# Kernel tuning notes

Measured on AMD Instinct MI355X. Metric: run time of the kernel, lower is better.

The kernel has to match this reference:

```python
import jax, jax.numpy as jnp
import numpy as np

DIM = 768
HEADS = 12
B, N = 1, 4096


def setup_inputs() -> dict:
    key = jax.random.key(0)
    k1, k2, k3 = jax.random.split(key, 3)
    x = jax.random.normal(k1, (B, N, DIM), dtype=jnp.float32)
    W_qkv = jax.random.normal(k2, (DIM, 3 * DIM), dtype=jnp.float32) * (DIM ** -0.5)
    W_out = jax.random.normal(k3, (DIM, DIM), dtype=jnp.float32) * (DIM ** -0.5)
    b_out = jnp.zeros((DIM,), dtype=jnp.float32)
    return {"x": x, "W_qkv": W_qkv, "W_out": W_out, "b_out": b_out}


def reference(x, W_qkv, W_out, b_out):
    b, n, dim = x.shape
    h = HEADS
    d = dim // h
    qkv = x @ W_qkv  # [b, n, 3*dim]
    q, k, v = jnp.split(qkv, 3, axis=-1)
    # 'b n (h d) -> b h n d'
    def to_heads(a):
        return a.reshape(b, n, h, d).transpose(0, 2, 1, 3)
    q, k, v = to_heads(q), to_heads(k), to_heads(v)
    # NOTE: original module computes self.scale but never applies it -> unscaled dots
    dots = jnp.einsum('bhid,bhjd->bhij', q, k)
    attn = jax.nn.softmax(dots, axis=-1)
    out = jnp.einsum('bhij,bhjd->bhid', attn, v)
    out = out.transpose(0, 2, 1, 3).reshape(b, n, dim)  # 'b h n d -> b n (h d)'
    return out @ W_out + b_out
```

## Files before the change

### kernel.cpp

```cpp
#include <hip/hip_runtime.h>

typedef unsigned short ushort_t;
typedef unsigned int uint_t;
typedef __bf16 bf16x8 __attribute__((ext_vector_type(8)));
typedef __bf16 bf16x4 __attribute__((ext_vector_type(4)));
typedef float f32x4 __attribute__((ext_vector_type(4)));
typedef ushort_t u16x4 __attribute__((ext_vector_type(4)));

#define NSEQ 4096
#define DIMM 768
#define NQKV 2304
#define HEADS 12
#define LOG2E 1.4426950408889634f

#if __has_builtin(__builtin_amdgcn_exp2f)
#define EXP2(x) __builtin_amdgcn_exp2f(x)
#else
#define EXP2(x) exp2f(x)
#endif


__device__ __forceinline__ ushort_t f2bf(float f) {
    uint_t u = __float_as_uint(f);
    u = u + 0x7fffu + ((u >> 16) & 1u);
    return (ushort_t)(u >> 16);
}
__device__ __forceinline__ f32x4 zero4() {
    f32x4 v = {0.f, 0.f, 0.f, 0.f};
    return v;
}

__global__ __launch_bounds__(256) void cvt_x_pack_kernel(const float* __restrict__ src,
                                                         ushort_t* __restrict__ dst) {
    int i = blockIdx.x * 256 + threadIdx.x;
    int row = i / (DIMM / 4);
    int k0 = (i - row * (DIMM / 4)) * 4;
    float4 v = *(const float4*)(&src[(size_t)row * DIMM + k0]);
    u16x4 p = { f2bf(v.x), f2bf(v.y), f2bf(v.z), f2bf(v.w) };
    size_t idx = ((size_t)(row >> 4) * (DIMM / 8) + (k0 >> 3)) * 128 + (row & 15) * 8 + (k0 & 7);
    *(u16x4*)(&dst[idx]) = p;
}

__global__ __launch_bounds__(256) void pack_w_kernel(
    const float* __restrict__ src, ushort_t* __restrict__ dst, int K, int N)
{
    __shared__ ushort_t Ls[64 * 72];
    const int t = threadIdx.x;
    const int bk = blockIdx.x * 64;
    const int bn = blockIdx.y * 64;
    const int tr = t >> 4, tc = t & 15;
#pragma unroll
    for (int i = 0; i < 4; ++i) {
        int r = tr + 16 * i;
        float4 v = *(const float4*)(&src[(size_t)(bk + r) * N + bn + tc * 4]);
        const float* vv = (const float*)&v;
#pragma unroll
        for (int j = 0; j < 4; ++j) Ls[(tc * 4 + j) * 72 + r] = f2bf(vv[j]);
    }
    __syncthreads();
    const int KB = K >> 3;
    const int n = t >> 2;
    const int ks = t & 3;
    const int gn = bn + n;
    size_t base = ((size_t)(gn >> 4) * KB + ((bk + ks * 16) >> 3)) * 128 + (gn & 15) * 8;
    *(uint4*)(&dst[base])       = *(const uint4*)(&Ls[n * 72 + ks * 16]);
    *(uint4*)(&dst[base + 128]) = *(const uint4*)(&Ls[n * 72 + ks * 16 + 8]);
}

__global__ __launch_bounds__(256) void qkv_gemm_kernel(
    const ushort_t* __restrict__ Ap, const ushort_t* __restrict__ Bp,
    ushort_t* __restrict__ Qp, ushort_t* __restrict__ Kp, ushort_t* __restrict__ Vp)
{
    const int t = threadIdx.x;
    const int lane = t & 63;
    const int w = t >> 6;
    const int m16 = lane & 15;
    const int g = lane >> 4;
    const int wrow = (w >> 1) * 64;
    const int wcol = (w & 1) * 64;
    const int bm = blockIdx.y * 128;
    const int bn = blockIdx.x * 128;
    const int amb = (bm + wrow) >> 4;
    const int bnb = (bn + wcol) >> 4;
    const int KB = DIMM / 8;
    const int which = bn / DIMM;

    f32x4 acc[4][4];
#pragma unroll
    for (int i = 0; i < 4; ++i)
#pragma unroll
        for (int j = 0; j < 4; ++j) acc[i][j] = zero4();

    if (which < 2) {
#pragma unroll 2
        for (int kt = 0; kt < 24; ++kt) {
            bf16x8 af[4], bfv[4];
#pragma unroll
            for (int mi = 0; mi < 4; ++mi)
                af[mi] = *(const bf16x8*)(&Ap[((size_t)(amb + mi) * KB + kt * 4 + g) * 128 + m16 * 8]);
#pragma unroll
            for (int nj = 0; nj < 4; ++nj)
                bfv[nj] = *(const bf16x8*)(&Bp[((size_t)(bnb + nj) * KB + kt * 4 + g) * 128 + m16 * 8]);
#pragma unroll
            for (int mi = 0; mi < 4; ++mi)
#pragma unroll
                for (int nj = 0; nj < 4; ++nj)
                    acc[mi][nj] = __builtin_amdgcn_mfma_f32_16x16x32_bf16(bfv[nj], af[mi], acc[mi][nj], 0, 0, 0);
        }
        ushort_t* dst = (which == 0) ? Qp : Kp;
        const float scale = (which == 0) ? LOG2E : 1.0f;
        const int cb = bn - which * DIMM + wcol;
        const int h = cb >> 6;
        const int ghi = g >> 1, glo = g & 1;
#pragma unroll
        for (int mi = 0; mi < 4; ++mi) {
            int sblk = amb + mi;
#pragma unroll
            for (int nj = 0; nj < 4; ++nj) {
                size_t idx = (((size_t)h * 256 + sblk) * 8 + nj * 2 + ghi) * 128 + m16 * 8 + glo * 4;
                u16x4 pk = { f2bf(acc[mi][nj][0] * scale), f2bf(acc[mi][nj][1] * scale),
                             f2bf(acc[mi][nj][2] * scale), f2bf(acc[mi][nj][3] * scale) };
                *(u16x4*)(&dst[idx]) = pk;
            }
        }
    } else {
#pragma unroll 2
        for (int kt = 0; kt < 24; ++kt) {
            bf16x8 af[4], bfv[4];
#pragma unroll
            for (int mi = 0; mi < 4; ++mi)
                af[mi] = *(const bf16x8*)(&Ap[((size_t)(amb + mi) * KB + kt * 4 + g) * 128 + m16 * 8]);
#pragma unroll
            for (int nj = 0; nj < 4; ++nj)
                bfv[nj] = *(const bf16x8*)(&Bp[((size_t)(bnb + nj) * KB + kt * 4 + g) * 128 + m16 * 8]);
#pragma unroll
            for (int mi = 0; mi < 4; ++mi)
#pragma unroll
                for (int nj = 0; nj < 4; ++nj)
                    acc[mi][nj] = __builtin_amdgcn_mfma_f32_16x16x32_bf16(af[mi], bfv[nj], acc[mi][nj], 0, 0, 0);
        }
        const int cb = bn - 2 * DIMM + wcol;
        const int h = cb >> 6;
        const int ghi = g >> 1, glo = g & 1;
        const int kb8 = (bm + wrow) >> 3;
#pragma unroll
        for (int mi = 0; mi < 4; ++mi) {
#pragma unroll
            for (int nj = 0; nj < 4; ++nj) {
                size_t idx = (((size_t)h * 512 + kb8 + mi * 2 + ghi) * 4 + nj) * 128 + m16 * 8 + glo * 4;
                u16x4 pk = { f2bf(acc[mi][nj][0]), f2bf(acc[mi][nj][1]),
                             f2bf(acc[mi][nj][2]), f2bf(acc[mi][nj][3]) };
                *(u16x4*)(&Vp[idx]) = pk;
            }
        }
    }
}

__global__ __launch_bounds__(256, 2) void attn_kernel(
    const ushort_t* __restrict__ Qp, const ushort_t* __restrict__ Kp,
    const ushort_t* __restrict__ Vp, float* __restrict__ Opart, float* __restrict__ Lpart,
    int niter)
{
    __shared__ ushort_t Ps[4][32 * 72];
    const int t = threadIdx.x;
    const int lane = t & 63;
    const int w = t >> 6;
    const int m16 = lane & 15;
    const int g = lane >> 4;
    const int h = blockIdx.y;
    const int half = blockIdx.z;
    const int qb = blockIdx.x * 128 + w * 32;
    const int qblk0 = qb >> 4;
    const int kblk0 = half * niter * 4;
    const int vblk0 = half * niter * 8;

    bf16x8 qf[2][2];
#pragma unroll
    for (int mi = 0; mi < 2; ++mi)
#pragma unroll
        for (int kd = 0; kd < 2; ++kd)
            qf[mi][kd] = *(const bf16x8*)(&Qp[(((size_t)h * 256 + qblk0 + mi) * 8 + kd * 4 + g) * 128 + m16 * 8]);

    const ushort_t* kpA = Kp + ((size_t)h * 256 + kblk0) * 1024 + g * 128 + m16 * 8;
    const ushort_t* kpB = kpA + 2048;
    const ushort_t* vpA = Vp + ((size_t)h * 512 + vblk0) * 512 + g * 512 + m16 * 8;
    const ushort_t* vpB = vpA + 2048;

    f32x4 oacc[2][4];
#pragma unroll
    for (int mi = 0; mi < 2; ++mi)
#pragma unroll
        for (int dj = 0; dj < 4; ++dj) oacc[mi][dj] = zero4();
    f32x4 lacc[2] = {zero4(), zero4()};

#pragma unroll 4
    for (int kt = 0; kt < niter; ++kt) {
        bf16x8 kf[4][2];
        kf[0][0] = *(const bf16x8*)(kpA);
        kf[0][1] = *(const bf16x8*)(kpA + 512);
        kf[1][0] = *(const bf16x8*)(kpA + 1024);
        kf[1][1] = *(const bf16x8*)(kpA + 1536);
        kf[2][0] = *(const bf16x8*)(kpB);
        kf[2][1] = *(const bf16x8*)(kpB + 512);
        kf[3][0] = *(const bf16x8*)(kpB + 1024);
        kf[3][1] = *(const bf16x8*)(kpB + 1536);
        bf16x8 vf[4][2];
#pragma unroll
        for (int dj = 0; dj < 4; ++dj) {
            vf[dj][0] = *(const bf16x8*)(vpA + dj * 128);
            vf[dj][1] = *(const bf16x8*)(vpB + dj * 128);
        }
        kpA += 4096; kpB += 4096; vpA += 4096; vpB += 4096;

#pragma unroll
        for (int nj = 0; nj < 4; ++nj) {
#pragma unroll
            for (int mi = 0; mi < 2; ++mi) {
                f32x4 st = zero4();
#pragma unroll
                for (int kd = 0; kd < 2; ++kd)
                    st = __builtin_amdgcn_mfma_f32_16x16x32_bf16(kf[nj][kd], qf[mi][kd], st, 0, 0, 0);
                f32x4 p;
#pragma unroll
                for (int r = 0; r < 4; ++r) p[r] = EXP2(st[r]);
                lacc[mi] += p;
                bf16x4 pk = { (__bf16)p[0], (__bf16)p[1], (__bf16)p[2], (__bf16)p[3] };
                *(bf16x4*)(&Ps[w][(mi * 16 + m16) * 72 + nj * 16 + g * 4]) = pk;
            }
        }
        bf16x8 pf[2][2];
#pragma unroll
        for (int mi = 0; mi < 2; ++mi)
#pragma unroll
            for (int kc = 0; kc < 2; ++kc)
                pf[mi][kc] = *(const bf16x8*)(&Ps[w][(mi * 16 + m16) * 72 + kc * 32 + g * 8]);
#pragma unroll
        for (int mi = 0; mi < 2; ++mi)
#pragma unroll
            for (int dj = 0; dj < 4; ++dj)
#pragma unroll
                for (int kc = 0; kc < 2; ++kc)
                    oacc[mi][dj] = __builtin_amdgcn_mfma_f32_16x16x32_bf16(pf[mi][kc], vf[dj][kc], oacc[mi][dj], 0, 0, 0);
    }

    float* Oph = Opart + (size_t)half * NSEQ * DIMM;
    float* Lph = Lpart + (size_t)half * HEADS * NSEQ + (size_t)h * NSEQ;
#pragma unroll
    for (int mi = 0; mi < 2; ++mi) {
        float l = (lacc[mi][0] + lacc[mi][1]) + (lacc[mi][2] + lacc[mi][3]);
        l += __shfl_xor(l, 16);
        l += __shfl_xor(l, 32);
        if (g == 0) Lph[qb + mi * 16 + m16] = l;
    }
#pragma unroll
    for (int mi = 0; mi < 2; ++mi) {
#pragma unroll
        for (int r = 0; r < 4; ++r) {
            int row = qb + mi * 16 + g * 4 + r;
#pragma unroll
            for (int dj = 0; dj < 4; ++dj)
                Oph[(size_t)row * DIMM + h * 64 + dj * 16 + m16] = oacc[mi][dj][r];
        }
    }
}

__global__ __launch_bounds__(256) void merge_kernel(
    const float* __restrict__ Opart, const float* __restrict__ Lpart,
    ushort_t* __restrict__ Xap, int nsplit)
{
    int i = blockIdx.x * 256 + threadIdx.x;
    int row = i / (DIMM / 4);
    int col0 = (i - row * (DIMM / 4)) * 4;
    int h = col0 >> 6;
    float l = 0.f;
    f32x4 o = zero4();
    for (int s = 0; s < nsplit; ++s) {
        l += Lpart[(size_t)s * HEADS * NSEQ + (size_t)h * NSEQ + row];
        f32x4 ov = *(const f32x4*)(&Opart[(size_t)s * NSEQ * DIMM + (size_t)row * DIMM + col0]);
        o += ov;
    }
    float inv = 1.0f / l;
    u16x4 p = { f2bf(o[0] * inv), f2bf(o[1] * inv), f2bf(o[2] * inv), f2bf(o[3] * inv) };
    size_t idx = ((size_t)(row >> 4) * (DIMM / 8) + (col0 >> 3)) * 128 + (row & 15) * 8 + (col0 & 7);
    *(u16x4*)(&Xap[idx]) = p;
}

__global__ __launch_bounds__(128) void out_gemm_kernel(
    const ushort_t* __restrict__ Ap, const ushort_t* __restrict__ Bp,
    const float* __restrict__ bias, float* __restrict__ out)
{
    const int t = threadIdx.x;
    const int lane = t & 63;
    const int w = t >> 6;
    const int m16 = lane & 15;
    const int g = lane >> 4;
    const int bm = blockIdx.y * 128;
    const int bn = blockIdx.x * 64;
    const int amb = (bm + w * 64) >> 4;
    const int bnb = bn >> 4;
    const int KB = DIMM / 8;

    f32x4 acc[4][4];
#pragma unroll
    for (int i = 0; i < 4; ++i)
#pragma unroll
        for (int j = 0; j < 4; ++j) acc[i][j] = zero4();

#pragma unroll 2
    for (int kt = 0; kt < 24; ++kt) {
        bf16x8 af[4], bfv[4];
#pragma unroll
        for (int mi = 0; mi < 4; ++mi)
            af[mi] = *(const bf16x8*)(&Ap[((size_t)(amb + mi) * KB + kt * 4 + g) * 128 + m16 * 8]);
#pragma unroll
        for (int nj = 0; nj < 4; ++nj)
            bfv[nj] = *(const bf16x8*)(&Bp[((size_t)(bnb + nj) * KB + kt * 4 + g) * 128 + m16 * 8]);
#pragma unroll
        for (int mi = 0; mi < 4; ++mi)
#pragma unroll
            for (int nj = 0; nj < 4; ++nj)
                acc[mi][nj] = __builtin_amdgcn_mfma_f32_16x16x32_bf16(af[mi], bfv[nj], acc[mi][nj], 0, 0, 0);
    }
#pragma unroll
    for (int mi = 0; mi < 4; ++mi) {
#pragma unroll
        for (int nj = 0; nj < 4; ++nj) {
            int col = bn + nj * 16 + m16;
            float bv = bias[col];
#pragma unroll
            for (int r = 0; r < 4; ++r) {
                int row = bm + w * 64 + mi * 16 + g * 4 + r;
                out[(size_t)row * DIMM + col] = acc[mi][nj][r] + bv;
            }
        }
    }
}

extern "C" void kernel_launch(void* const* d_in, const int* in_sizes, int n_in,
                              void* d_out, int out_size, void* d_ws, size_t ws_size,
                              hipStream_t stream) {
    (void)in_sizes; (void)n_in; (void)out_size;
    const float* X    = (const float*)d_in[0];
    const float* Wqkv = (const float*)d_in[1];
    const float* Wout = (const float*)d_in[2];
    const float* bout = (const float*)d_in[3];
    float* out = (float*)d_out;

    const size_t TSZ = (size_t)NSEQ * DIMM;
    const size_t fixed = TSZ * 2 * 5 + (size_t)NQKV * DIMM * 2 + (size_t)DIMM * DIMM * 2;
    const size_t per_split = TSZ * 4 + (size_t)HEADS * NSEQ * 4;
    const int nsplit = (ws_size >= fixed + 4 * per_split) ? 4 : 2;

    unsigned char* p = (unsigned char*)d_ws;
    ushort_t* Ap  = (ushort_t*)p; p += TSZ * 2;
    ushort_t* Wqp = (ushort_t*)p; p += (size_t)NQKV * DIMM * 2;
    ushort_t* Wop = (ushort_t*)p; p += (size_t)DIMM * DIMM * 2;
    ushort_t* Qp  = (ushort_t*)p; p += TSZ * 2;
    ushort_t* Kp  = (ushort_t*)p; p += TSZ * 2;
    ushort_t* Vp  = (ushort_t*)p; p += TSZ * 2;
    ushort_t* Xap = (ushort_t*)p; p += TSZ * 2;
    float* Opart  = (float*)p;    p += (size_t)nsplit * TSZ * 4;
    float* Lpart  = (float*)p;

    const int niter = (NSEQ / 64) / nsplit;

    cvt_x_pack_kernel<<<TSZ / 4 / 256, 256, 0, stream>>>(X, Ap);
    pack_w_kernel<<<dim3(DIMM / 64, NQKV / 64), 256, 0, stream>>>(Wqkv, Wqp, DIMM, NQKV);
    pack_w_kernel<<<dim3(DIMM / 64, DIMM / 64), 256, 0, stream>>>(Wout, Wop, DIMM, DIMM);
    qkv_gemm_kernel<<<dim3(NQKV / 128, NSEQ / 128), 256, 0, stream>>>(Ap, Wqp, Qp, Kp, Vp);
    attn_kernel<<<dim3(NSEQ / 128, HEADS, nsplit), 256, 0, stream>>>(Qp, Kp, Vp, Opart, Lpart, niter);
    merge_kernel<<<TSZ / 4 / 256, 256, 0, stream>>>(Opart, Lpart, Xap, nsplit);
    out_gemm_kernel<<<dim3(DIMM / 64, NSEQ / 128), 128, 0, stream>>>(Xap, Wop, bout, out);
}
```

Measured before the change: 210.5 us.

## Fuse prep kernels, widen GEMM warp tiles, use single-wave attention blocks with fixed split

```diff
diff --git a/kernel.cpp b/kernel.cpp
--- a/kernel.cpp
+++ b/kernel.cpp
@@ -30,24 +30,10 @@
     return v;
 }
 
-__global__ __launch_bounds__(256) void cvt_x_pack_kernel(const float* __restrict__ src,
-                                                         ushort_t* __restrict__ dst) {
-    int i = blockIdx.x * 256 + threadIdx.x;
-    int row = i / (DIMM / 4);
-    int k0 = (i - row * (DIMM / 4)) * 4;
-    float4 v = *(const float4*)(&src[(size_t)row * DIMM + k0]);
-    u16x4 p = { f2bf(v.x), f2bf(v.y), f2bf(v.z), f2bf(v.w) };
-    size_t idx = ((size_t)(row >> 4) * (DIMM / 8) + (k0 >> 3)) * 128 + (row & 15) * 8 + (k0 & 7);
-    *(u16x4*)(&dst[idx]) = p;
-}
-
-__global__ __launch_bounds__(256) void pack_w_kernel(
-    const float* __restrict__ src, ushort_t* __restrict__ dst, int K, int N)
-{
-    __shared__ ushort_t Ls[64 * 72];
-    const int t = threadIdx.x;
-    const int bk = blockIdx.x * 64;
-    const int bn = blockIdx.y * 64;
+__device__ __forceinline__ void pack_w_tile(const float* __restrict__ src,
+                                            ushort_t* __restrict__ dst,
+                                            int K, int N, int bk, int bn, int t,
+                                            ushort_t* Ls) {
     const int tr = t >> 4, tc = t & 15;
 #pragma unroll
     for (int i = 0; i < 4; ++i) {
@@ -67,7 +53,44 @@
     *(uint4*)(&dst[base + 128]) = *(const uint4*)(&Ls[n * 72 + ks * 16 + 8]);
 }
 
-__global__ __launch_bounds__(256) void qkv_gemm_kernel(
+#define CVT_BLOCKS   3072
+#define PW1_BLOCKS   (12 * 36)
+#define PW2_BLOCKS   (12 * 12)
+
+__global__ __launch_bounds__(256) void prep_kernel(
+    const float* __restrict__ X, const float* __restrict__ Wqkv, const float* __restrict__ Wout,
+    ushort_t* __restrict__ Ap, ushort_t* __restrict__ Wqp, ushort_t* __restrict__ Wop)
+{
+    __shared__ ushort_t Ls[64 * 72];
+    const int b = blockIdx.x;
+    const int t = threadIdx.x;
+    if (b < CVT_BLOCKS) {
+        int i = b * 256 + t;
+        int row = i / (DIMM / 4);
+        int k0 = (i - row * (DIMM / 4)) * 4;
+        float4 v = *(const float4*)(&X[(size_t)row * DIMM + k0]);
+        u16x4 p = { f2bf(v.x), f2bf(v.y), f2bf(v.z), f2bf(v.w) };
+        size_t idx = ((size_t)(row >> 4) * (DIMM / 8) + (k0 >> 3)) * 128 + (row & 15) * 8 + (k0 & 7);
+        *(u16x4*)(&Ap[idx]) = p;
+    } else if (b < CVT_BLOCKS + PW1_BLOCKS) {
+        int j = b - CVT_BLOCKS;
+        pack_w_tile(Wqkv, Wqp, DIMM, NQKV, (j % 12) * 64, (j / 12) * 64, t, Ls);
+    } else {
+        int j = b - CVT_BLOCKS - PW1_BLOCKS;
+        pack_w_tile(Wout, Wop, DIMM, DIMM, (j % 12) * 64, (j / 12) * 64, t, Ls);
+    }
+}
+
+#define QKV_LOAD8(af, bfv, kt) do {                                                           \
+    _Pragma("unroll")                                                                         \
+    for (int mi = 0; mi < 4; ++mi)                                                            \
+        af[mi] = *(const bf16x8*)(&Ap[((size_t)(amb + mi) * KB + (kt) * 4 + g) * 128 + m16 * 8]); \
+    _Pragma("unroll")                                                                         \
+    for (int nj = 0; nj < 8; ++nj)                                                            \
+        bfv[nj] = *(const bf16x8*)(&Bp[((size_t)(bnb + nj) * KB + (kt) * 4 + g) * 128 + m16 * 8]); \
+} while (0)
+
+__global__ __launch_bounds__(128, 2) void qkv_gemm_kernel(
     const ushort_t* __restrict__ Ap, const ushort_t* __restrict__ Bp,
     ushort_t* __restrict__ Qp, ushort_t* __restrict__ Kp, ushort_t* __restrict__ Vp)
 {
@@ -76,78 +99,64 @@
     const int w = t >> 6;
     const int m16 = lane & 15;
     const int g = lane >> 4;
-    const int wrow = (w >> 1) * 64;
-    const int wcol = (w & 1) * 64;
-    const int bm = blockIdx.y * 128;
-    const int bn = blockIdx.x * 128;
-    const int amb = (bm + wrow) >> 4;
+    const int bm = blockIdx.y * 64;
+    const int bn = blockIdx.x * 256;
+    const int wcol = w * 128;
+    const int amb = bm >> 4;
     const int bnb = (bn + wcol) >> 4;
     const int KB = DIMM / 8;
     const int which = bn / DIMM;
-
-    f32x4 acc[4][4];
+    const int ghi = g >> 1, glo = g & 1;
+
+    f32x4 acc[4][8];
 #pragma unroll
     for (int i = 0; i < 4; ++i)
 #pragma unroll
-        for (int j = 0; j < 4; ++j) acc[i][j] = zero4();
+        for (int j = 0; j < 8; ++j) acc[i][j] = zero4();
 
     if (which < 2) {
-#pragma unroll 2
         for (int kt = 0; kt < 24; ++kt) {
-            bf16x8 af[4], bfv[4];
+            bf16x8 af[4], bfv[8];
+            QKV_LOAD8(af, bfv, kt);
 #pragma unroll
             for (int mi = 0; mi < 4; ++mi)
-                af[mi] = *(const bf16x8*)(&Ap[((size_t)(amb + mi) * KB + kt * 4 + g) * 128 + m16 * 8]);
-#pragma unroll
-            for (int nj = 0; nj < 4; ++nj)
-                bfv[nj] = *(const bf16x8*)(&Bp[((size_t)(bnb + nj) * KB + kt * 4 + g) * 128 + m16 * 8]);
-#pragma unroll
-            for (int mi = 0; mi < 4; ++mi)
-#pragma unroll
-                for (int nj = 0; nj < 4; ++nj)
+#pragma unroll
+                for (int nj = 0; nj < 8; ++nj)
                     acc[mi][nj] = __builtin_amdgcn_mfma_f32_16x16x32_bf16(bfv[nj], af[mi], acc[mi][nj], 0, 0, 0);
         }
         ushort_t* dst = (which == 0) ? Qp : Kp;
         const float scale = (which == 0) ? LOG2E : 1.0f;
         const int cb = bn - which * DIMM + wcol;
-        const int h = cb >> 6;
-        const int ghi = g >> 1, glo = g & 1;
 #pragma unroll
         for (int mi = 0; mi < 4; ++mi) {
             int sblk = amb + mi;
 #pragma unroll
-            for (int nj = 0; nj < 4; ++nj) {
-                size_t idx = (((size_t)h * 256 + sblk) * 8 + nj * 2 + ghi) * 128 + m16 * 8 + glo * 4;
+            for (int nj = 0; nj < 8; ++nj) {
+                int h = (cb >> 6) + (nj >> 2);
+                size_t idx = (((size_t)h * 256 + sblk) * 8 + (nj & 3) * 2 + ghi) * 128 + m16 * 8 + glo * 4;
                 u16x4 pk = { f2bf(acc[mi][nj][0] * scale), f2bf(acc[mi][nj][1] * scale),
                              f2bf(acc[mi][nj][2] * scale), f2bf(acc[mi][nj][3] * scale) };
                 *(u16x4*)(&dst[idx]) = pk;
             }
         }
     } else {
-#pragma unroll 2
         for (int kt = 0; kt < 24; ++kt) {
-            bf16x8 af[4], bfv[4];
+            bf16x8 af[4], bfv[8];
+            QKV_LOAD8(af, bfv, kt);
 #pragma unroll
             for (int mi = 0; mi < 4; ++mi)
-                af[mi] = *(const bf16x8*)(&Ap[((size_t)(amb + mi) * KB + kt * 4 + g) * 128 + m16 * 8]);
-#pragma unroll
-            for (int nj = 0; nj < 4; ++nj)
-                bfv[nj] = *(const bf16x8*)(&Bp[((size_t)(bnb + nj) * KB + kt * 4 + g) * 128 + m16 * 8]);
-#pragma unroll
-            for (int mi = 0; mi < 4; ++mi)
-#pragma unroll
-                for (int nj = 0; nj < 4; ++nj)
+#pragma unroll
+                for (int nj = 0; nj < 8; ++nj)
                     acc[mi][nj] = __builtin_amdgcn_mfma_f32_16x16x32_bf16(af[mi], bfv[nj], acc[mi][nj], 0, 0, 0);
         }
         const int cb = bn - 2 * DIMM + wcol;
-        const int h = cb >> 6;
-        const int ghi = g >> 1, glo = g & 1;
-        const int kb8 = (bm + wrow) >> 3;
+        const int kb8 = bm >> 3;
 #pragma unroll
         for (int mi = 0; mi < 4; ++mi) {
 #pragma unroll
-            for (int nj = 0; nj < 4; ++nj) {
-                size_t idx = (((size_t)h * 512 + kb8 + mi * 2 + ghi) * 4 + nj) * 128 + m16 * 8 + glo * 4;
+            for (int nj = 0; nj < 8; ++nj) {
+                int h = (cb >> 6) + (nj >> 2);
+                size_t idx = (((size_t)h * 512 + kb8 + mi * 2 + ghi) * 4 + (nj & 3)) * 128 + m16 * 8 + glo * 4;
                 u16x4 pk = { f2bf(acc[mi][nj][0]), f2bf(acc[mi][nj][1]),
                              f2bf(acc[mi][nj][2]), f2bf(acc[mi][nj][3]) };
                 *(u16x4*)(&Vp[idx]) = pk;
@@ -156,27 +165,25 @@
     }
 }
 
-__global__ __launch_bounds__(256, 2) void attn_kernel(
+__global__ __launch_bounds__(64, 2) void attn_kernel(
     const ushort_t* __restrict__ Qp, const ushort_t* __restrict__ Kp,
     const ushort_t* __restrict__ Vp, float* __restrict__ Opart, float* __restrict__ Lpart,
     int niter)
 {
-    __shared__ ushort_t Ps[4][32 * 72];
-    const int t = threadIdx.x;
-    const int lane = t & 63;
-    const int w = t >> 6;
+    __shared__ ushort_t Ps[64 * 72];
+    const int lane = threadIdx.x & 63;
     const int m16 = lane & 15;
     const int g = lane >> 4;
     const int h = blockIdx.y;
     const int half = blockIdx.z;
-    const int qb = blockIdx.x * 128 + w * 32;
+    const int qb = blockIdx.x * 64;
     const int qblk0 = qb >> 4;
     const int kblk0 = half * niter * 4;
     const int vblk0 = half * niter * 8;
 
-    bf16x8 qf[2][2];
-#pragma unroll
-    for (int mi = 0; mi < 2; ++mi)
+    bf16x8 qf[4][2];
+#pragma unroll
+    for (int mi = 0; mi < 4; ++mi)
 #pragma unroll
         for (int kd = 0; kd < 2; ++kd)
             qf[mi][kd] = *(const bf16x8*)(&Qp[(((size_t)h * 256 + qblk0 + mi) * 8 + kd * 4 + g) * 128 + m16 * 8]);
@@ -186,14 +193,13 @@
     const ushort_t* vpA = Vp + ((size_t)h * 512 + vblk0) * 512 + g * 512 + m16 * 8;
     const ushort_t* vpB = vpA + 2048;
 
-    f32x4 oacc[2][4];
-#pragma unroll
-    for (int mi = 0; mi < 2; ++mi)
+    f32x4 oacc[4][4];
+#pragma unroll
+    for (int mi = 0; mi < 4; ++mi)
 #pragma unroll
         for (int dj = 0; dj < 4; ++dj) oacc[mi][dj] = zero4();
-    f32x4 lacc[2] = {zero4(), zero4()};
-
-#pragma unroll 4
+    f32x4 lacc[4] = {zero4(), zero4(), zero4(), zero4()};
+
     for (int kt = 0; kt < niter; ++kt) {
         bf16x8 kf[4][2];
         kf[0][0] = *(const bf16x8*)(kpA);
@@ -215,45 +221,41 @@
 #pragma unroll
         for (int nj = 0; nj < 4; ++nj) {
 #pragma unroll
-            for (int mi = 0; mi < 2; ++mi) {
+            for (int mi = 0; mi < 4; ++mi) {
                 f32x4 st = zero4();
-#pragma unroll
-                for (int kd = 0; kd < 2; ++kd)
-                    st = __builtin_amdgcn_mfma_f32_16x16x32_bf16(kf[nj][kd], qf[mi][kd], st, 0, 0, 0);
+                st = __builtin_amdgcn_mfma_f32_16x16x32_bf16(kf[nj][0], qf[mi][0], st, 0, 0, 0);
+                st = __builtin_amdgcn_mfma_f32_16x16x32_bf16(kf[nj][1], qf[mi][1], st, 0, 0, 0);
                 f32x4 p;
 #pragma unroll
                 for (int r = 0; r < 4; ++r) p[r] = EXP2(st[r]);
                 lacc[mi] += p;
                 bf16x4 pk = { (__bf16)p[0], (__bf16)p[1], (__bf16)p[2], (__bf16)p[3] };
-                *(bf16x4*)(&Ps[w][(mi * 16 + m16) * 72 + nj * 16 + g * 4]) = pk;
-            }
-        }
-        bf16x8 pf[2][2];
-#pragma unroll
-        for (int mi = 0; mi < 2; ++mi)
-#pragma unroll
-            for (int kc = 0; kc < 2; ++kc)
-                pf[mi][kc] = *(const bf16x8*)(&Ps[w][(mi * 16 + m16) * 72 + kc * 32 + g * 8]);
-#pragma unroll
-        for (int mi = 0; mi < 2; ++mi)
-#pragma unroll
-            for (int dj = 0; dj < 4; ++dj)
-#pragma unroll
-                for (int kc = 0; kc < 2; ++kc)
-                    oacc[mi][dj] = __builtin_amdgcn_mfma_f32_16x16x32_bf16(pf[mi][kc], vf[dj][kc], oacc[mi][dj], 0, 0, 0);
+                *(bf16x4*)(&Ps[(mi * 16 + m16) * 72 + nj * 16 + g * 4]) = pk;
+            }
+        }
+#pragma unroll
+        for (int mi = 0; mi < 4; ++mi) {
+            bf16x8 pf0 = *(const bf16x8*)(&Ps[(mi * 16 + m16) * 72 + g * 8]);
+            bf16x8 pf1 = *(const bf16x8*)(&Ps[(mi * 16 + m16) * 72 + 32 + g * 8]);
+#pragma unroll
+            for (int dj = 0; dj < 4; ++dj) {
+                oacc[mi][dj] = __builtin_amdgcn_mfma_f32_16x16x32_bf16(pf0, vf[dj][0], oacc[mi][dj], 0, 0, 0);
+                oacc[mi][dj] = __builtin_amdgcn_mfma_f32_16x16x32_bf16(pf1, vf[dj][1], oacc[mi][dj], 0, 0, 0);
+            }
+        }
     }
 
     float* Oph = Opart + (size_t)half * NSEQ * DIMM;
     float* Lph = Lpart + (size_t)half * HEADS * NSEQ + (size_t)h * NSEQ;
 #pragma unroll
-    for (int mi = 0; mi < 2; ++mi) {
+    for (int mi = 0; mi < 4; ++mi) {
         float l = (lacc[mi][0] + lacc[mi][1]) + (lacc[mi][2] + lacc[mi][3]);
         l += __shfl_xor(l, 16);
         l += __shfl_xor(l, 32);
         if (g == 0) Lph[qb + mi * 16 + m16] = l;
     }
 #pragma unroll
-    for (int mi = 0; mi < 2; ++mi) {
+    for (int mi = 0; mi < 4; ++mi) {
 #pragma unroll
         for (int r = 0; r < 4; ++r) {
             int row = qb + mi * 16 + g * 4 + r;
@@ -285,7 +287,7 @@
     *(u16x4*)(&Xap[idx]) = p;
 }
 
-__global__ __launch_bounds__(128) void out_gemm_kernel(
+__global__ __launch_bounds__(128, 2) void out_gemm_kernel(
     const ushort_t* __restrict__ Ap, const ushort_t* __restrict__ Bp,
     const float* __restrict__ bias, float* __restrict__ out)
 {
@@ -295,36 +297,30 @@
     const int m16 = lane & 15;
     const int g = lane >> 4;
     const int bm = blockIdx.y * 128;
-    const int bn = blockIdx.x * 64;
+    const int bn = blockIdx.x * 128;
     const int amb = (bm + w * 64) >> 4;
     const int bnb = bn >> 4;
     const int KB = DIMM / 8;
 
-    f32x4 acc[4][4];
+    f32x4 acc[4][8];
 #pragma unroll
     for (int i = 0; i < 4; ++i)
 #pragma unroll
-        for (int j = 0; j < 4; ++j) acc[i][j] = zero4();
-
-#pragma unroll 2
+        for (int j = 0; j < 8; ++j) acc[i][j] = zero4();
+
     for (int kt = 0; kt < 24; ++kt) {
-        bf16x8 af[4], bfv[4];
+        bf16x8 af[4], bfv[8];
+        QKV_LOAD8(af, bfv, kt);
 #pragma unroll
         for (int mi = 0; mi < 4; ++mi)
-            af[mi] = *(const bf16x8*)(&Ap[((size_t)(amb + mi) * KB + kt * 4 + g) * 128 + m16 * 8]);
-#pragma unroll
-        for (int nj = 0; nj < 4; ++nj)
-            bfv[nj] = *(const bf16x8*)(&Bp[((size_t)(bnb + nj) * KB + kt * 4 + g) * 128 + m16 * 8]);
-#pragma unroll
-        for (int mi = 0; mi < 4; ++mi)
-#pragma unroll
-            for (int nj = 0; nj < 4; ++nj)
+#pragma unroll
+            for (int nj = 0; nj < 8; ++nj)
                 acc[mi][nj] = __builtin_amdgcn_mfma_f32_16x16x32_bf16(af[mi], bfv[nj], acc[mi][nj], 0, 0, 0);
     }
 #pragma unroll
     for (int mi = 0; mi < 4; ++mi) {
 #pragma unroll
-        for (int nj = 0; nj < 4; ++nj) {
+        for (int nj = 0; nj < 8; ++nj) {
             int col = bn + nj * 16 + m16;
             float bv = bias[col];
 #pragma unroll
@@ -339,7 +335,7 @@
 extern "C" void kernel_launch(void* const* d_in, const int* in_sizes, int n_in,
                               void* d_out, int out_size, void* d_ws, size_t ws_size,
                               hipStream_t stream) {
-    (void)in_sizes; (void)n_in; (void)out_size;
+    (void)in_sizes; (void)n_in; (void)out_size; (void)ws_size;
     const float* X    = (const float*)d_in[0];
     const float* Wqkv = (const float*)d_in[1];
     const float* Wout = (const float*)d_in[2];
@@ -347,9 +343,7 @@
     float* out = (float*)d_out;
 
     const size_t TSZ = (size_t)NSEQ * DIMM;
-    const size_t fixed = TSZ * 2 * 5 + (size_t)NQKV * DIMM * 2 + (size_t)DIMM * DIMM * 2;
-    const size_t per_split = TSZ * 4 + (size_t)HEADS * NSEQ * 4;
-    const int nsplit = (ws_size >= fixed + 4 * per_split) ? 4 : 2;
+    const int nsplit = 2;
 
     unsigned char* p = (unsigned char*)d_ws;
     ushort_t* Ap  = (ushort_t*)p; p += TSZ * 2;
@@ -364,11 +358,9 @@
 
     const int niter = (NSEQ / 64) / nsplit;
 
-    cvt_x_pack_kernel<<<TSZ / 4 / 256, 256, 0, stream>>>(X, Ap);
-    pack_w_kernel<<<dim3(DIMM / 64, NQKV / 64), 256, 0, stream>>>(Wqkv, Wqp, DIMM, NQKV);
-    pack_w_kernel<<<dim3(DIMM / 64, DIMM / 64), 256, 0, stream>>>(Wout, Wop, DIMM, DIMM);
-    qkv_gemm_kernel<<<dim3(NQKV / 128, NSEQ / 128), 256, 0, stream>>>(Ap, Wqp, Qp, Kp, Vp);
-    attn_kernel<<<dim3(NSEQ / 128, HEADS, nsplit), 256, 0, stream>>>(Qp, Kp, Vp, Opart, Lpart, niter);
+    prep_kernel<<<CVT_BLOCKS + PW1_BLOCKS + PW2_BLOCKS, 256, 0, stream>>>(X, Wqkv, Wout, Ap, Wqp, Wop);
+    qkv_gemm_kernel<<<dim3(NQKV / 256, NSEQ / 64), 128, 0, stream>>>(Ap, Wqp, Qp, Kp, Vp);
+    attn_kernel<<<dim3(NSEQ / 64, HEADS, nsplit), 64, 0, stream>>>(Qp, Kp, Vp, Opart, Lpart, niter);
     merge_kernel<<<TSZ / 4 / 256, 256, 0, stream>>>(Opart, Lpart, Xap, nsplit);
-    out_gemm_kernel<<<dim3(DIMM / 64, NSEQ / 128), 128, 0, stream>>>(Xap, Wop, bout, out);
-}
+    out_gemm_kernel<<<dim3(DIMM / 128, NSEQ / 128), 128, 0, stream>>>(Xap, Wop, bout, out);
+}
```

Result: slower. 240.9 us (+14.4%).

## Fuse prep kernels, double-buffer QKV loads, raise attention occupancy, shrink out-GEMM tiles

Applied to the files above, without the earlier changes.

```diff
diff --git a/kernel.cpp b/kernel.cpp
--- a/kernel.cpp
+++ b/kernel.cpp
@@ -30,24 +30,10 @@
     return v;
 }
 
-__global__ __launch_bounds__(256) void cvt_x_pack_kernel(const float* __restrict__ src,
-                                                         ushort_t* __restrict__ dst) {
-    int i = blockIdx.x * 256 + threadIdx.x;
-    int row = i / (DIMM / 4);
-    int k0 = (i - row * (DIMM / 4)) * 4;
-    float4 v = *(const float4*)(&src[(size_t)row * DIMM + k0]);
-    u16x4 p = { f2bf(v.x), f2bf(v.y), f2bf(v.z), f2bf(v.w) };
-    size_t idx = ((size_t)(row >> 4) * (DIMM / 8) + (k0 >> 3)) * 128 + (row & 15) * 8 + (k0 & 7);
-    *(u16x4*)(&dst[idx]) = p;
-}
-
-__global__ __launch_bounds__(256) void pack_w_kernel(
-    const float* __restrict__ src, ushort_t* __restrict__ dst, int K, int N)
-{
-    __shared__ ushort_t Ls[64 * 72];
-    const int t = threadIdx.x;
-    const int bk = blockIdx.x * 64;
-    const int bn = blockIdx.y * 64;
+__device__ __forceinline__ void pack_w_tile(const float* __restrict__ src,
+                                            ushort_t* __restrict__ dst,
+                                            int K, int N, int bk, int bn, int t,
+                                            ushort_t* Ls) {
     const int tr = t >> 4, tc = t & 15;
 #pragma unroll
     for (int i = 0; i < 4; ++i) {
@@ -66,6 +52,43 @@
     *(uint4*)(&dst[base])       = *(const uint4*)(&Ls[n * 72 + ks * 16]);
     *(uint4*)(&dst[base + 128]) = *(const uint4*)(&Ls[n * 72 + ks * 16 + 8]);
 }
+
+#define CVT_BLOCKS   3072
+#define PW1_BLOCKS   (12 * 36)
+#define PW2_BLOCKS   (12 * 12)
+
+__global__ __launch_bounds__(256) void prep_kernel(
+    const float* __restrict__ X, const float* __restrict__ Wqkv, const float* __restrict__ Wout,
+    ushort_t* __restrict__ Ap, ushort_t* __restrict__ Wqp, ushort_t* __restrict__ Wop)
+{
+    __shared__ ushort_t Ls[64 * 72];
+    const int b = blockIdx.x;
+    const int t = threadIdx.x;
+    if (b < CVT_BLOCKS) {
+        int i = b * 256 + t;
+        int row = i / (DIMM / 4);
+        int k0 = (i - row * (DIMM / 4)) * 4;
+        float4 v = *(const float4*)(&X[(size_t)row * DIMM + k0]);
+        u16x4 p = { f2bf(v.x), f2bf(v.y), f2bf(v.z), f2bf(v.w) };
+        size_t idx = ((size_t)(row >> 4) * (DIMM / 8) + (k0 >> 3)) * 128 + (row & 15) * 8 + (k0 & 7);
+        *(u16x4*)(&Ap[idx]) = p;
+    } else if (b < CVT_BLOCKS + PW1_BLOCKS) {
+        int j = b - CVT_BLOCKS;
+        pack_w_tile(Wqkv, Wqp, DIMM, NQKV, (j % 12) * 64, (j / 12) * 64, t, Ls);
+    } else {
+        int j = b - CVT_BLOCKS - PW1_BLOCKS;
+        pack_w_tile(Wout, Wop, DIMM, DIMM, (j % 12) * 64, (j / 12) * 64, t, Ls);
+    }
+}
+
+#define QKV_LOAD(af, bfv, kt) do {                                                            \
+    _Pragma("unroll")                                                                         \
+    for (int mi = 0; mi < 4; ++mi)                                                            \
+        af[mi] = *(const bf16x8*)(&Ap[((size_t)(amb + mi) * KB + (kt) * 4 + g) * 128 + m16 * 8]); \
+    _Pragma("unroll")                                                                         \
+    for (int nj = 0; nj < 4; ++nj)                                                            \
+        bfv[nj] = *(const bf16x8*)(&Bp[((size_t)(bnb + nj) * KB + (kt) * 4 + g) * 128 + m16 * 8]); \
+} while (0)
 
 __global__ __launch_bounds__(256) void qkv_gemm_kernel(
     const ushort_t* __restrict__ Ap, const ushort_t* __restrict__ Bp,
@@ -91,21 +114,23 @@
 #pragma unroll
         for (int j = 0; j < 4; ++j) acc[i][j] = zero4();
 
+    bf16x8 af0[4], bf0[4], af1[4], bf1[4];
+    QKV_LOAD(af0, bf0, 0);
+
     if (which < 2) {
-#pragma unroll 2
-        for (int kt = 0; kt < 24; ++kt) {
-            bf16x8 af[4], bfv[4];
+        for (int kt = 0; kt < 24; kt += 2) {
+            QKV_LOAD(af1, bf1, kt + 1);
 #pragma unroll
             for (int mi = 0; mi < 4; ++mi)
-                af[mi] = *(const bf16x8*)(&Ap[((size_t)(amb + mi) * KB + kt * 4 + g) * 128 + m16 * 8]);
-#pragma unroll
-            for (int nj = 0; nj < 4; ++nj)
-                bfv[nj] = *(const bf16x8*)(&Bp[((size_t)(bnb + nj) * KB + kt * 4 + g) * 128 + m16 * 8]);
+#pragma unroll
+                for (int nj = 0; nj < 4; ++nj)
+                    acc[mi][nj] = __builtin_amdgcn_mfma_f32_16x16x32_bf16(bf0[nj], af0[mi], acc[mi][nj], 0, 0, 0);
+            if (kt + 2 < 24) QKV_LOAD(af0, bf0, kt + 2);
 #pragma unroll
             for (int mi = 0; mi < 4; ++mi)
 #pragma unroll
                 for (int nj = 0; nj < 4; ++nj)
-                    acc[mi][nj] = __builtin_amdgcn_mfma_f32_16x16x32_bf16(bfv[nj], af[mi], acc[mi][nj], 0, 0, 0);
+                    acc[mi][nj] = __builtin_amdgcn_mfma_f32_16x16x32_bf16(bf1[nj], af1[mi], acc[mi][nj], 0, 0, 0);
         }
         ushort_t* dst = (which == 0) ? Qp : Kp;
         const float scale = (which == 0) ? LOG2E : 1.0f;
@@ -124,20 +149,19 @@
             }
         }
     } else {
-#pragma unroll 2
-        for (int kt = 0; kt < 24; ++kt) {
-            bf16x8 af[4], bfv[4];
+        for (int kt = 0; kt < 24; kt += 2) {
+            QKV_LOAD(af1, bf1, kt + 1);
 #pragma unroll
             for (int mi = 0; mi < 4; ++mi)
-                af[mi] = *(const bf16x8*)(&Ap[((size_t)(amb + mi) * KB + kt * 4 + g) * 128 + m16 * 8]);
-#pragma unroll
-            for (int nj = 0; nj < 4; ++nj)
-                bfv[nj] = *(const bf16x8*)(&Bp[((size_t)(bnb + nj) * KB + kt * 4 + g) * 128 + m16 * 8]);
+#pragma unroll
+                for (int nj = 0; nj < 4; ++nj)
+                    acc[mi][nj] = __builtin_amdgcn_mfma_f32_16x16x32_bf16(af0[mi], bf0[nj], acc[mi][nj], 0, 0, 0);
+            if (kt + 2 < 24) QKV_LOAD(af0, bf0, kt + 2);
 #pragma unroll
             for (int mi = 0; mi < 4; ++mi)
 #pragma unroll
                 for (int nj = 0; nj < 4; ++nj)
-                    acc[mi][nj] = __builtin_amdgcn_mfma_f32_16x16x32_bf16(af[mi], bfv[nj], acc[mi][nj], 0, 0, 0);
+                    acc[mi][nj] = __builtin_amdgcn_mfma_f32_16x16x32_bf16(af1[mi], bf1[nj], acc[mi][nj], 0, 0, 0);
         }
         const int cb = bn - 2 * DIMM + wcol;
         const int h = cb >> 6;
@@ -156,7 +180,7 @@
     }
 }
 
-__global__ __launch_bounds__(256, 2) void attn_kernel(
+__global__ __launch_bounds__(256, 4) void attn_kernel(
     const ushort_t* __restrict__ Qp, const ushort_t* __restrict__ Kp,
     const ushort_t* __restrict__ Vp, float* __restrict__ Opart, float* __restrict__ Lpart,
     int niter)
@@ -285,51 +309,49 @@
     *(u16x4*)(&Xap[idx]) = p;
 }
 
-__global__ __launch_bounds__(128) void out_gemm_kernel(
+__global__ __launch_bounds__(64, 4) void out_gemm_kernel(
     const ushort_t* __restrict__ Ap, const ushort_t* __restrict__ Bp,
     const float* __restrict__ bias, float* __restrict__ out)
 {
-    const int t = threadIdx.x;
-    const int lane = t & 63;
-    const int w = t >> 6;
+    const int lane = threadIdx.x & 63;
     const int m16 = lane & 15;
     const int g = lane >> 4;
-    const int bm = blockIdx.y * 128;
+    const int bm = blockIdx.y * 32;
     const int bn = blockIdx.x * 64;
-    const int amb = (bm + w * 64) >> 4;
+    const int amb = bm >> 4;
     const int bnb = bn >> 4;
     const int KB = DIMM / 8;
 
-    f32x4 acc[4][4];
-#pragma unroll
-    for (int i = 0; i < 4; ++i)
+    f32x4 acc[2][4];
+#pragma unroll
+    for (int i = 0; i < 2; ++i)
 #pragma unroll
         for (int j = 0; j < 4; ++j) acc[i][j] = zero4();
 
 #pragma unroll 2
     for (int kt = 0; kt < 24; ++kt) {
-        bf16x8 af[4], bfv[4];
-#pragma unroll
-        for (int mi = 0; mi < 4; ++mi)
+        bf16x8 af[2], bfv[4];
+#pragma unroll
+        for (int mi = 0; mi < 2; ++mi)
             af[mi] = *(const bf16x8*)(&Ap[((size_t)(amb + mi) * KB + kt * 4 + g) * 128 + m16 * 8]);
 #pragma unroll
         for (int nj = 0; nj < 4; ++nj)
             bfv[nj] = *(const bf16x8*)(&Bp[((size_t)(bnb + nj) * KB + kt * 4 + g) * 128 + m16 * 8]);
 #pragma unroll
-        for (int mi = 0; mi < 4; ++mi)
+        for (int mi = 0; mi < 2; ++mi)
 #pragma unroll
             for (int nj = 0; nj < 4; ++nj)
                 acc[mi][nj] = __builtin_amdgcn_mfma_f32_16x16x32_bf16(af[mi], bfv[nj], acc[mi][nj], 0, 0, 0);
     }
 #pragma unroll
-    for (int mi = 0; mi < 4; ++mi) {
+    for (int mi = 0; mi < 2; ++mi) {
 #pragma unroll
         for (int nj = 0; nj < 4; ++nj) {
             int col = bn + nj * 16 + m16;
             float bv = bias[col];
 #pragma unroll
             for (int r = 0; r < 4; ++r) {
-                int row = bm + w * 64 + mi * 16 + g * 4 + r;
+                int row = bm + mi * 16 + g * 4 + r;
                 out[(size_t)row * DIMM + col] = acc[mi][nj][r] + bv;
             }
         }
@@ -364,11 +386,9 @@
 
     const int niter = (NSEQ / 64) / nsplit;
 
-    cvt_x_pack_kernel<<<TSZ / 4 / 256, 256, 0, stream>>>(X, Ap);
-    pack_w_kernel<<<dim3(DIMM / 64, NQKV / 64), 256, 0, stream>>>(Wqkv, Wqp, DIMM, NQKV);
-    pack_w_kernel<<<dim3(DIMM / 64, DIMM / 64), 256, 0, stream>>>(Wout, Wop, DIMM, DIMM);
+    prep_kernel<<<CVT_BLOCKS + PW1_BLOCKS + PW2_BLOCKS, 256, 0, stream>>>(X, Wqkv, Wout, Ap, Wqp, Wop);
     qkv_gemm_kernel<<<dim3(NQKV / 128, NSEQ / 128), 256, 0, stream>>>(Ap, Wqp, Qp, Kp, Vp);
     attn_kernel<<<dim3(NSEQ / 128, HEADS, nsplit), 256, 0, stream>>>(Qp, Kp, Vp, Opart, Lpart, niter);
     merge_kernel<<<TSZ / 4 / 256, 256, 0, stream>>>(Opart, Lpart, Xap, nsplit);
-    out_gemm_kernel<<<dim3(DIMM / 64, NSEQ / 128), 128, 0, stream>>>(Xap, Wop, bout, out);
-}
+    out_gemm_kernel<<<dim3(DIMM / 64, NSEQ / 32), 64, 0, stream>>>(Xap, Wop, bout, out);
+}
```

Result: faster. 204.3 us (-2.9%).
